# Kernel tuning notes

Measured on AMD Instinct MI355X. Metric: run time of the kernel, lower is better.

The kernel has to match this reference:

```python
import jax, jax.numpy as jnp
import numpy as np

N = 1536
F = 64          # in_features
F_IN = F + 1    # include_adj adds adjacency channel
OUT = 64


def setup_inputs() -> dict:
    key = jax.random.key(0)
    k1, k2, k3, k4 = jax.random.split(key, 4)
    feat = jax.random.normal(k1, (N, F), dtype=jnp.float32)
    adj = jax.random.uniform(k2, (N, N), dtype=jnp.float32)
    # nn.Linear init: U(-1/sqrt(fan_in), 1/sqrt(fan_in))
    bound = 1.0 / np.sqrt(F_IN)
    W = jax.random.uniform(k3, (OUT, F_IN), minval=-bound, maxval=bound, dtype=jnp.float32)
    b = jax.random.uniform(k4, (OUT,), minval=-bound, maxval=bound, dtype=jnp.float32)
    return {"feat": feat, "adj": adj, "W": W, "b": b}


def reference(feat, adj, W, b):
    # pairwise abs-diff via broadcasting (no repeat): [N, N, F]
    feat_diff = jnp.abs(feat[None, :, :] - feat[:, None, :])
    # concat adjacency as extra channel -> [N, N, F+1], then flatten rows
    x = jnp.concatenate([feat_diff, adj[:, :, None]], axis=2).reshape(N * N, F_IN)
    # Linear: x @ W.T + b -> [N*N, OUT]
    return x @ W.T + b
```

## Files before the change

### kernel.cpp

```cpp
#include <hip/hip_runtime.h>
#include <hip/hip_bf16.h>

#define N_NODES 1536
#define NF 64
#define NOUT 64
#define FIN 65
#define TI 24

typedef __bf16 bf16x8 __attribute__((ext_vector_type(8)));
typedef float f32x4 __attribute__((ext_vector_type(4)));

__global__ __launch_bounds__(256, 3)
void edge_gcn_mfma(const float* __restrict__ feat,
                   const float* __restrict__ adj,
                   const float* __restrict__ W,
                   const float* __restrict__ b,
                   float* __restrict__ out)
{
    const int tid  = threadIdx.x;
    const int lane = tid & 63;
    const int wv   = tid >> 6;
    const int l15  = lane & 15;
    const int lg   = lane >> 4;

    const int i0 = blockIdx.y * TI;
    const int j0 = blockIdx.x * 128;
    const int jw = j0 + wv * 32;

    __shared__ float lds[8192];
    __shared__ float fslab[TI * NF];
    __shared__ float aslab[TI * 128];
    float* const lbase = lds + wv * 2048;

#pragma unroll
    for (int h = 0; h < 2; ++h) {
        const int idx = h * 256 + tid;
        if (idx < 384) {
            const int row = idx >> 4;
            const int col = (idx & 15) * 4;
            *reinterpret_cast<f32x4*>(&fslab[row * NF + col]) =
                *reinterpret_cast<const f32x4*>(
                    &feat[(size_t)(i0 + row) * NF + col]);
        }
    }
#pragma unroll
    for (int h = 0; h < 3; ++h) {
        const int idx = h * 256 + tid;
        const int row = idx >> 5;
        const int col = (idx & 31) * 4;
        *reinterpret_cast<f32x4*>(&aslab[row * 128 + col]) =
            *reinterpret_cast<const f32x4*>(
                &adj[(size_t)(i0 + row) * N_NODES + j0 + col]);
    }

    bf16x8 afrag[2][4];
#pragma unroll
    for (int kk = 0; kk < 2; ++kk) {
#pragma unroll
        for (int mo = 0; mo < 4; ++mo) {
            const float* wp = W + (mo * 16 + l15) * FIN + kk * 32 + lg * 8;
#pragma unroll
            for (int e = 0; e < 8; ++e) afrag[kk][mo][e] = (__bf16)wp[e];
        }
    }

    float fjr[2][2][8];
#pragma unroll
    for (int n = 0; n < 2; ++n) {
        const float* fjrow = feat + (jw + n * 16 + l15) * NF;
#pragma unroll
        for (int kk = 0; kk < 2; ++kk)
#pragma unroll
            for (int e = 0; e < 8; ++e)
                fjr[n][kk][e] = fjrow[kk * 32 + lg * 8 + e];
    }

    float wlB[4], bvB[4];
#pragma unroll
    for (int r = 0; r < 4; ++r) {
        wlB[r] = W[(l15 * 4 + r) * FIN + NF];
        bvB[r] = b[l15 * 4 + r];
    }

    __syncthreads();

#pragma unroll 1
    for (int ii = 0; ii < TI; ++ii) {
        const int i = i0 + ii;

        float fi[2][8];
#pragma unroll
        for (int kk = 0; kk < 2; ++kk) {
            const float* fp = &fslab[ii * NF + kk * 32 + lg * 8];
#pragma unroll
            for (int e = 0; e < 8; ++e) fi[kk][e] = fp[e];
        }

        f32x4 acc[4][2];
#pragma unroll
        for (int mo = 0; mo < 4; ++mo)
#pragma unroll
            for (int n = 0; n < 2; ++n)
                acc[mo][n] = (f32x4){0.f, 0.f, 0.f, 0.f};

#pragma unroll
        for (int n = 0; n < 2; ++n) {
#pragma unroll
            for (int kk = 0; kk < 2; ++kk) {
                bf16x8 bfrag;
#pragma unroll
                for (int e = 0; e < 8; ++e)
                    bfrag[e] = (__bf16)fabsf(fjr[n][kk][e] - fi[kk][e]);
#pragma unroll
                for (int mo = 0; mo < 4; ++mo)
                    acc[mo][n] = __builtin_amdgcn_mfma_f32_16x16x32_bf16(
                        afrag[kk][mo], bfrag, acc[mo][n], 0, 0, 0);
            }
        }

#pragma unroll
        for (int n = 0; n < 2; ++n) {
            const int jrow = n * 16 + l15;
#pragma unroll
            for (int mo = 0; mo < 4; ++mo) {
                const int swz = (mo * 16 + lg * 4) ^ ((l15 & 7) << 2);
                *reinterpret_cast<f32x4*>(lbase + jrow * 64 + swz) = acc[mo][n];
            }
        }

#pragma unroll
        for (int t = 0; t < 8; ++t) {
            const int jr = t * 4 + lg;
            const int oo = l15 * 4;
            f32x4 v = *reinterpret_cast<const f32x4*>(
                lbase + jr * 64 + (oo ^ ((jr & 7) << 2)));
            const float av = aslab[ii * 128 + wv * 32 + jr];
#pragma unroll
            for (int r = 0; r < 4; ++r)
                v[r] = v[r] + av * wlB[r] + bvB[r];
            float* op = out + ((size_t)i * N_NODES + jw + jr) * NOUT + oo;
            *reinterpret_cast<f32x4*>(op) = v;
        }
    }
}

extern "C" void kernel_launch(void* const* d_in, const int* in_sizes, int n_in,
                              void* d_out, int out_size, void* d_ws, size_t ws_size,
                              hipStream_t stream) {
    const float* feat = (const float*)d_in[0];
    const float* adj  = (const float*)d_in[1];
    const float* W    = (const float*)d_in[2];
    const float* b    = (const float*)d_in[3];
    float* out = (float*)d_out;

    dim3 grid(N_NODES / 128, N_NODES / TI);
    dim3 block(256);
    edge_gcn_mfma<<<grid, block, 0, stream>>>(feat, adj, W, b, out);
}
```

Before: 122.5 us.

## Software-pipeline output stores behind next row's MFMA and pre-convert features to bf16

```diff
diff --git a/kernel.cpp b/kernel.cpp
--- a/kernel.cpp
+++ b/kernel.cpp
@@ -64,7 +64,7 @@
         }
     }
 
-    float fjr[2][2][8];
+    bf16x8 fjrb[2][2];
 #pragma unroll
     for (int n = 0; n < 2; ++n) {
         const float* fjrow = feat + (jw + n * 16 + l15) * NF;
@@ -72,7 +72,7 @@
         for (int kk = 0; kk < 2; ++kk)
 #pragma unroll
             for (int e = 0; e < 8; ++e)
-                fjr[n][kk][e] = fjrow[kk * 32 + lg * 8 + e];
+                fjrb[n][kk][e] = (__bf16)fjrow[kk * 32 + lg * 8 + e];
     }
 
     float wlB[4], bvB[4];
@@ -84,16 +84,13 @@
 
     __syncthreads();
 
-#pragma unroll 1
-    for (int ii = 0; ii < TI; ++ii) {
-        const int i = i0 + ii;
-
-        float fi[2][8];
+    auto compute_eA = [&](int ii) {
+        bf16x8 fib[2];
 #pragma unroll
         for (int kk = 0; kk < 2; ++kk) {
             const float* fp = &fslab[ii * NF + kk * 32 + lg * 8];
 #pragma unroll
-            for (int e = 0; e < 8; ++e) fi[kk][e] = fp[e];
+            for (int e = 0; e < 8; ++e) fib[kk][e] = (__bf16)fp[e];
         }
 
         f32x4 acc[4][2];
@@ -110,7 +107,8 @@
                 bf16x8 bfrag;
 #pragma unroll
                 for (int e = 0; e < 8; ++e)
-                    bfrag[e] = (__bf16)fabsf(fjr[n][kk][e] - fi[kk][e]);
+                    bfrag[e] = (__bf16)fabsf((float)fjrb[n][kk][e] -
+                                             (float)fib[kk][e]);
 #pragma unroll
                 for (int mo = 0; mo < 4; ++mo)
                     acc[mo][n] = __builtin_amdgcn_mfma_f32_16x16x32_bf16(
@@ -127,7 +125,9 @@
                 *reinterpret_cast<f32x4*>(lbase + jrow * 64 + swz) = acc[mo][n];
             }
         }
+    };
 
+    auto read_fin = [&](f32x4* S, int ii) {
 #pragma unroll
         for (int t = 0; t < 8; ++t) {
             const int jr = t * 4 + lg;
@@ -138,10 +138,30 @@
 #pragma unroll
             for (int r = 0; r < 4; ++r)
                 v[r] = v[r] + av * wlB[r] + bvB[r];
-            float* op = out + ((size_t)i * N_NODES + jw + jr) * NOUT + oo;
-            *reinterpret_cast<f32x4*>(op) = v;
+            S[t] = v;
         }
+    };
+
+    auto store_tile = [&](const f32x4* S, int ii) {
+        float* const orow =
+            out + ((size_t)(i0 + ii) * N_NODES + jw) * NOUT + l15 * 4;
+#pragma unroll
+        for (int t = 0; t < 8; ++t)
+            *reinterpret_cast<f32x4*>(orow + (t * 4 + lg) * NOUT) = S[t];
+    };
+
+    f32x4 S0[8], S1[8];
+#pragma unroll 1
+    for (int ii = 0; ii < TI; ii += 2) {
+        compute_eA(ii);
+        if (ii) store_tile(S1, ii - 1);
+        read_fin(S0, ii);
+
+        compute_eA(ii + 1);
+        store_tile(S0, ii);
+        read_fin(S1, ii + 1);
     }
+    store_tile(S1, TI - 1);
 }
 
 extern "C" void kernel_launch(void* const* d_in, const int* in_sizes, int n_in,
```

New measurement: 124.0 us. No clear change (+1.2%).

## Retile work so each wave owns i-rows and streams j features from LDS

Applied to the files above, without the earlier changes.

```diff
diff --git a/kernel.cpp b/kernel.cpp
--- a/kernel.cpp
+++ b/kernel.cpp
@@ -5,12 +5,13 @@
 #define NF 64
 #define NOUT 64
 #define FIN 65
-#define TI 24
+#define TIB 12
+#define TIW 3
 
 typedef __bf16 bf16x8 __attribute__((ext_vector_type(8)));
 typedef float f32x4 __attribute__((ext_vector_type(4)));
 
-__global__ __launch_bounds__(256, 3)
+__global__ __launch_bounds__(256, 2)
 void edge_gcn_mfma(const float* __restrict__ feat,
                    const float* __restrict__ adj,
                    const float* __restrict__ W,
@@ -23,57 +24,58 @@
     const int l15  = lane & 15;
     const int lg   = lane >> 4;
 
-    const int i0 = blockIdx.y * TI;
+    const int i0 = blockIdx.y * TIB;
     const int j0 = blockIdx.x * 128;
-    const int jw = j0 + wv * 32;
+    const int iw = i0 + wv * TIW;
 
-    __shared__ float lds[8192];
-    __shared__ float fslab[TI * NF];
-    __shared__ float aslab[TI * 128];
+    __shared__ float  lds[8192];
+    __shared__ __bf16 fjslab[128 * NF];
+    __shared__ __bf16 fslab[TIB * NF];
+    __shared__ float  aslab[TIB * 128];
     float* const lbase = lds + wv * 2048;
 
+#pragma unroll
+    for (int h = 0; h < 4; ++h) {
+        const int idx = h * 256 + tid;
+        const int r = idx >> 3, s = idx & 7;
+        const float* fp = feat + (size_t)(j0 + r) * NF + s * 8;
+        f32x4 lo = *reinterpret_cast<const f32x4*>(fp);
+        f32x4 hi = *reinterpret_cast<const f32x4*>(fp + 4);
+        bf16x8 v;
+#pragma unroll
+        for (int e = 0; e < 4; ++e) { v[e] = (__bf16)lo[e]; v[e+4] = (__bf16)hi[e]; }
+        *reinterpret_cast<bf16x8*>(&fjslab[r * NF + ((s ^ (r & 7)) * 8)]) = v;
+    }
+    if (tid < 96) {
+        const int r = tid >> 3, s = tid & 7;
+        const float* fp = feat + (size_t)(i0 + r) * NF + s * 8;
+        f32x4 lo = *reinterpret_cast<const f32x4*>(fp);
+        f32x4 hi = *reinterpret_cast<const f32x4*>(fp + 4);
+        bf16x8 v;
+#pragma unroll
+        for (int e = 0; e < 4; ++e) { v[e] = (__bf16)lo[e]; v[e+4] = (__bf16)hi[e]; }
+        *reinterpret_cast<bf16x8*>(&fslab[r * NF + s * 8]) = v;
+    }
 #pragma unroll
     for (int h = 0; h < 2; ++h) {
         const int idx = h * 256 + tid;
         if (idx < 384) {
-            const int row = idx >> 4;
-            const int col = (idx & 15) * 4;
-            *reinterpret_cast<f32x4*>(&fslab[row * NF + col]) =
+            const int row = idx >> 5, col = (idx & 31) * 4;
+            *reinterpret_cast<f32x4*>(&aslab[row * 128 + col]) =
                 *reinterpret_cast<const f32x4*>(
-                    &feat[(size_t)(i0 + row) * NF + col]);
+                    &adj[(size_t)(i0 + row) * N_NODES + j0 + col]);
         }
-    }
-#pragma unroll
-    for (int h = 0; h < 3; ++h) {
-        const int idx = h * 256 + tid;
-        const int row = idx >> 5;
-        const int col = (idx & 31) * 4;
-        *reinterpret_cast<f32x4*>(&aslab[row * 128 + col]) =
-            *reinterpret_cast<const f32x4*>(
-                &adj[(size_t)(i0 + row) * N_NODES + j0 + col]);
     }
 
     bf16x8 afrag[2][4];
 #pragma unroll
-    for (int kk = 0; kk < 2; ++kk) {
+    for (int kk = 0; kk < 2; ++kk)
 #pragma unroll
         for (int mo = 0; mo < 4; ++mo) {
             const float* wp = W + (mo * 16 + l15) * FIN + kk * 32 + lg * 8;
 #pragma unroll
             for (int e = 0; e < 8; ++e) afrag[kk][mo][e] = (__bf16)wp[e];
         }
-    }
-
-    float fjr[2][2][8];
-#pragma unroll
-    for (int n = 0; n < 2; ++n) {
-        const float* fjrow = feat + (jw + n * 16 + l15) * NF;
-#pragma unroll
-        for (int kk = 0; kk < 2; ++kk)
-#pragma unroll
-            for (int e = 0; e < 8; ++e)
-                fjr[n][kk][e] = fjrow[kk * 32 + lg * 8 + e];
-    }
 
     float wlB[4], bvB[4];
 #pragma unroll
@@ -85,61 +87,75 @@
     __syncthreads();
 
 #pragma unroll 1
-    for (int ii = 0; ii < TI; ++ii) {
-        const int i = i0 + ii;
+    for (int ii = 0; ii < TIW; ++ii) {
+        const int i = iw + ii;
 
-        float fi[2][8];
+        bf16x8 fib[2];
 #pragma unroll
-        for (int kk = 0; kk < 2; ++kk) {
-            const float* fp = &fslab[ii * NF + kk * 32 + lg * 8];
-#pragma unroll
-            for (int e = 0; e < 8; ++e) fi[kk][e] = fp[e];
-        }
+        for (int kk = 0; kk < 2; ++kk)
+            fib[kk] = *reinterpret_cast<const bf16x8*>(
+                &fslab[(wv * TIW + ii) * NF + kk * 32 + lg * 8]);
 
-        f32x4 acc[4][2];
-#pragma unroll
-        for (int mo = 0; mo < 4; ++mo)
+#pragma unroll 1
+        for (int t = 0; t < 4; ++t) {
+            bf16x8 fj[2][2];
 #pragma unroll
             for (int n = 0; n < 2; ++n)
-                acc[mo][n] = (f32x4){0.f, 0.f, 0.f, 0.f};
+#pragma unroll
+                for (int kk = 0; kk < 2; ++kk) {
+                    const int row  = t * 32 + n * 16 + l15;
+                    const int slot = (kk * 4 + lg) ^ (row & 7);
+                    fj[n][kk] = *reinterpret_cast<const bf16x8*>(
+                        &fjslab[row * NF + slot * 8]);
+                }
+
+            f32x4 acc[4][2];
+#pragma unroll
+            for (int mo = 0; mo < 4; ++mo)
+#pragma unroll
+                for (int n = 0; n < 2; ++n)
+                    acc[mo][n] = (f32x4){0.f, 0.f, 0.f, 0.f};
 
 #pragma unroll
-        for (int n = 0; n < 2; ++n) {
+            for (int n = 0; n < 2; ++n)
 #pragma unroll
-            for (int kk = 0; kk < 2; ++kk) {
-                bf16x8 bfrag;
+                for (int kk = 0; kk < 2; ++kk) {
+                    bf16x8 bfrag;
 #pragma unroll
-                for (int e = 0; e < 8; ++e)
-                    bfrag[e] = (__bf16)fabsf(fjr[n][kk][e] - fi[kk][e]);
+                    for (int e = 0; e < 8; ++e)
+                        bfrag[e] = (__bf16)fabsf((float)fj[n][kk][e] -
+                                                 (float)fib[kk][e]);
 #pragma unroll
-                for (int mo = 0; mo < 4; ++mo)
-                    acc[mo][n] = __builtin_amdgcn_mfma_f32_16x16x32_bf16(
-                        afrag[kk][mo], bfrag, acc[mo][n], 0, 0, 0);
-            }
-        }
+                    for (int mo = 0; mo < 4; ++mo)
+                        acc[mo][n] = __builtin_amdgcn_mfma_f32_16x16x32_bf16(
+                            afrag[kk][mo], bfrag, acc[mo][n], 0, 0, 0);
+                }
 
 #pragma unroll
-        for (int n = 0; n < 2; ++n) {
-            const int jrow = n * 16 + l15;
+            for (int n = 0; n < 2; ++n) {
+                const int jrow = n * 16 + l15;
 #pragma unroll
-            for (int mo = 0; mo < 4; ++mo) {
-                const int swz = (mo * 16 + lg * 4) ^ ((l15 & 7) << 2);
-                *reinterpret_cast<f32x4*>(lbase + jrow * 64 + swz) = acc[mo][n];
+                for (int mo = 0; mo < 4; ++mo) {
+                    const int swz = (mo * 16 + lg * 4) ^ ((l15 & 7) << 2);
+                    *reinterpret_cast<f32x4*>(lbase + jrow * 64 + swz) =
+                        acc[mo][n];
+                }
             }
-        }
 
 #pragma unroll
-        for (int t = 0; t < 8; ++t) {
-            const int jr = t * 4 + lg;
-            const int oo = l15 * 4;
-            f32x4 v = *reinterpret_cast<const f32x4*>(
-                lbase + jr * 64 + (oo ^ ((jr & 7) << 2)));
-            const float av = aslab[ii * 128 + wv * 32 + jr];
+            for (int tt = 0; tt < 8; ++tt) {
+                const int jr = tt * 4 + lg;
+                const int oo = l15 * 4;
+                f32x4 v = *reinterpret_cast<const f32x4*>(
+                    lbase + jr * 64 + (oo ^ ((jr & 7) << 2)));
+                const float av = aslab[(wv * TIW + ii) * 128 + t * 32 + jr];
 #pragma unroll
-            for (int r = 0; r < 4; ++r)
-                v[r] = v[r] + av * wlB[r] + bvB[r];
-            float* op = out + ((size_t)i * N_NODES + jw + jr) * NOUT + oo;
-            *reinterpret_cast<f32x4*>(op) = v;
+                for (int r = 0; r < 4; ++r)
+                    v[r] = v[r] + av * wlB[r] + bvB[r];
+                float* op = out +
+                    ((size_t)i * N_NODES + j0 + t * 32 + jr) * NOUT + oo;
+                *reinterpret_cast<f32x4*>(op) = v;
+            }
         }
     }
 }
@@ -153,7 +169,7 @@
     const float* b    = (const float*)d_in[3];
     float* out = (float*)d_out;
 
-    dim3 grid(N_NODES / 128, N_NODES / TI);
+    dim3 grid(N_NODES / 128, N_NODES / TIB);
     dim3 block(256);
     edge_gcn_mfma<<<grid, block, 0, stream>>>(feat, adj, W, b, out);
 }
```

After: 127.4 us. 3.9% more time.
